# Kernel optimization log

Measured on AMD Instinct MI355X. Metric: run time of the kernel, lower is better.

Reference implementation:

```python
import jax, jax.numpy as jnp
import numpy as np

R_CUT = 2.5
N_BASIS = 8
BOX_SIZE = 10.0


def radial_encode(r, n, r_cut):
    """Gaussian radial basis on squared distance r: (...,) -> (..., n).
    Centers spread over [0, r_cut], width r_cut/n. (Helper source not given;
    this is the standard RBF encode used in such MD graph nets.)"""
    mu = jnp.linspace(0.0, r_cut, n, dtype=r.dtype)        # (n,)
    sigma = r_cut / n
    d = r[..., None] - mu                                   # (..., n)
    return jnp.exp(-0.5 * (d / sigma) ** 2)


def setup_inputs() -> dict:
    key = jax.random.key(0)
    k1, k2 = jax.random.split(key)
    batch, nodes, deg = 8, 20000, 32
    pos = jax.random.uniform(k1, (batch, nodes, 3), dtype=jnp.float32) * BOX_SIZE
    box = jnp.full((3,), BOX_SIZE, dtype=jnp.float32)
    nbr_idx = jax.random.randint(k2, (nodes, deg), 0, nodes, dtype=jnp.int64)
    return {"pos": pos, "box": box, "nbr_idx": nbr_idx}


def reference(pos, box, nbr_idx):
    # pos: (B, N, 3); box: (3,); nbr_idx: (N, deg)
    ang_box = box / (2.0 * jnp.pi)                          # (3,)
    # edges_read: gather neighbor positions -> (B, N, deg, 3)
    nbr_pos = pos[:, nbr_idx]                               # (B, N, deg, 3)
    edges = nbr_pos - pos[:, :, None]                       # relative displacement
    # periodic-box sin wrap
    edges = ang_box * jnp.sin(edges / ang_box)
    r = jnp.sum(edges ** 2, axis=-1)                        # (B, N, deg) squared dist
    x = radial_encode(r, N_BASIS, R_CUT)                    # (B, N, deg, 8)
    xv = x[..., None] * edges[..., None, :]                 # (B, N, deg, 8, 3) outer product
    # edges_reduce: sum over neighbor axis
    y = jnp.sum(x, axis=2)                                  # (B, N, 8)
    yv = jnp.sum(xv, axis=2)                                # (B, N, 8, 3)
    return (y, yv)
```

## Files before the change

### kernel.cpp

```cpp
#include <hip/hip_runtime.h>

static constexpr int BATCH = 8;
static constexpr int NODES = 20000;
static constexpr int DEG   = 32;
static constexpr int NB    = 8;

#if defined(__has_builtin) && __has_builtin(__builtin_amdgcn_exp2f)
#define EXP2F(x) __builtin_amdgcn_exp2f(x)
#else
#define EXP2F(x) exp2f(x)
#endif

static constexpr float C1 = -7.3865986f;
static constexpr float C2 = 5.2761417f;

__global__ __launch_bounds__(256)
void pack_pos_kernel(const float* __restrict__ pos, float4* __restrict__ pos4) {
    const int t = blockIdx.x * blockDim.x + threadIdx.x;
    if (t >= BATCH * NODES) return;
    pos4[t] = make_float4(pos[3 * t + 0], pos[3 * t + 1], pos[3 * t + 2], 0.0f);
}

__global__ __launch_bounds__(256)
void graph_embed_kernel(const float4* __restrict__ pos4,
                        const float* __restrict__ box,
                        const int*   __restrict__ nbr,
                        float* __restrict__ out)
{
    const int t = blockIdx.x * blockDim.x + threadIdx.x;
    if (t >= BATCH * NODES) return;
    const int b = t / NODES;
    const int i = t - b * NODES;

    const float inv2pi = 0.15915494309189535f;
    const float ab0 = box[0] * inv2pi;
    const float ab1 = box[1] * inv2pi;
    const float ab2 = box[2] * inv2pi;
    const float ia0 = 1.0f / ab0;
    const float ia1 = 1.0f / ab1;
    const float ia2 = 1.0f / ab2;

    float h[NB - 1];
#pragma unroll
    for (int k = 0; k < NB - 1; ++k)
        h[k] = __expf(-0.6530612245f * (float)(2 * k + 1));

    const float4* __restrict__ pb = pos4 + (size_t)b * NODES;
    const float4 p = pb[i];

    float y0[NB], v0[NB], v1[NB], v2[NB];
#pragma unroll
    for (int k = 0; k < NB; ++k) { y0[k] = 0.f; v0[k] = 0.f; v1[k] = 0.f; v2[k] = 0.f; }

    const int4* __restrict__ row = (const int4*)(nbr + (size_t)i * DEG);

    int4 idx = row[0];
    float4 q0 = pb[idx.x], q1 = pb[idx.y], q2 = pb[idx.z], q3 = pb[idx.w];

#pragma unroll
    for (int grp = 0; grp < DEG / 4; ++grp) {
        float4 n0, n1, n2, n3;
        if (grp + 1 < DEG / 4) {
            const int4 nidx = row[grp + 1];
            n0 = pb[nidx.x]; n1 = pb[nidx.y]; n2 = pb[nidx.z]; n3 = pb[nidx.w];
        }
        const float4 qs[4] = { q0, q1, q2, q3 };
#pragma unroll
        for (int jj = 0; jj < 4; ++jj) {
            const float4 q = qs[jj];
            const float e0 = ab0 * __sinf((q.x - p.x) * ia0);
            const float e1 = ab1 * __sinf((q.y - p.y) * ia1);
            const float e2 = ab2 * __sinf((q.z - p.z) * ia2);
            const float r  = fmaf(e0, e0, fmaf(e1, e1, e2 * e2));

            const float g = EXP2F(r * C2);
            float x = EXP2F(r * r * C1);
#pragma unroll
            for (int k = 0; k < NB; ++k) {
                y0[k] += x;
                v0[k] = fmaf(x, e0, v0[k]);
                v1[k] = fmaf(x, e1, v1[k]);
                v2[k] = fmaf(x, e2, v2[k]);
                if (k < NB - 1) x = x * g * h[k];
            }
        }
        q0 = n0; q1 = n1; q2 = n2; q3 = n3;
    }

    float* __restrict__ yptr = out + (size_t)t * NB;
    *(float4*)(yptr + 0) = make_float4(y0[0], y0[1], y0[2], y0[3]);
    *(float4*)(yptr + 4) = make_float4(y0[4], y0[5], y0[6], y0[7]);

    float* __restrict__ vptr = out + (size_t)BATCH * NODES * NB + (size_t)t * (NB * 3);
    *(float4*)(vptr +  0) = make_float4(v0[0], v1[0], v2[0], v0[1]);
    *(float4*)(vptr +  4) = make_float4(v1[1], v2[1], v0[2], v1[2]);
    *(float4*)(vptr +  8) = make_float4(v2[2], v0[3], v1[3], v2[3]);
    *(float4*)(vptr + 12) = make_float4(v0[4], v1[4], v2[4], v0[5]);
    *(float4*)(vptr + 16) = make_float4(v1[5], v2[5], v0[6], v1[6]);
    *(float4*)(vptr + 20) = make_float4(v2[6], v0[7], v1[7], v2[7]);
}

__global__ __launch_bounds__(256)
void graph_embed_fallback_kernel(const float* __restrict__ pos,
                                 const float* __restrict__ box,
                                 const int*   __restrict__ nbr,
                                 float* __restrict__ out)
{
    const int t = blockIdx.x * blockDim.x + threadIdx.x;
    if (t >= BATCH * NODES) return;
    const int b = t / NODES;
    const int i = t - b * NODES;

    const float inv2pi = 0.15915494309189535f;
    const float ab0 = box[0] * inv2pi, ab1 = box[1] * inv2pi, ab2 = box[2] * inv2pi;
    const float ia0 = 1.0f / ab0, ia1 = 1.0f / ab1, ia2 = 1.0f / ab2;

    float h[NB - 1];
#pragma unroll
    for (int k = 0; k < NB - 1; ++k)
        h[k] = __expf(-0.6530612245f * (float)(2 * k + 1));

    const float* __restrict__ pb = pos + (size_t)b * NODES * 3;
    const float p0 = pb[3 * i + 0], p1 = pb[3 * i + 1], p2 = pb[3 * i + 2];

    float y0[NB], v0[NB], v1[NB], v2[NB];
#pragma unroll
    for (int k = 0; k < NB; ++k) { y0[k] = 0.f; v0[k] = 0.f; v1[k] = 0.f; v2[k] = 0.f; }

    const int* __restrict__ row = nbr + (size_t)i * DEG;
#pragma unroll 4
    for (int j = 0; j < DEG; ++j) {
        const int idx = row[j];
        const float* __restrict__ q = pb + (size_t)idx * 3;
        const float e0 = ab0 * __sinf((q[0] - p0) * ia0);
        const float e1 = ab1 * __sinf((q[1] - p1) * ia1);
        const float e2 = ab2 * __sinf((q[2] - p2) * ia2);
        const float r  = fmaf(e0, e0, fmaf(e1, e1, e2 * e2));
        const float g = EXP2F(r * C2);
        float x = EXP2F(r * r * C1);
#pragma unroll
        for (int k = 0; k < NB; ++k) {
            y0[k] += x;
            v0[k] = fmaf(x, e0, v0[k]);
            v1[k] = fmaf(x, e1, v1[k]);
            v2[k] = fmaf(x, e2, v2[k]);
            if (k < NB - 1) x = x * g * h[k];
        }
    }

    float* __restrict__ yptr = out + (size_t)t * NB;
    *(float4*)(yptr + 0) = make_float4(y0[0], y0[1], y0[2], y0[3]);
    *(float4*)(yptr + 4) = make_float4(y0[4], y0[5], y0[6], y0[7]);
    float* __restrict__ vptr = out + (size_t)BATCH * NODES * NB + (size_t)t * (NB * 3);
    *(float4*)(vptr +  0) = make_float4(v0[0], v1[0], v2[0], v0[1]);
    *(float4*)(vptr +  4) = make_float4(v1[1], v2[1], v0[2], v1[2]);
    *(float4*)(vptr +  8) = make_float4(v2[2], v0[3], v1[3], v2[3]);
    *(float4*)(vptr + 12) = make_float4(v0[4], v1[4], v2[4], v0[5]);
    *(float4*)(vptr + 16) = make_float4(v1[5], v2[5], v0[6], v1[6]);
    *(float4*)(vptr + 20) = make_float4(v2[6], v0[7], v1[7], v2[7]);
}

extern "C" void kernel_launch(void* const* d_in, const int* in_sizes, int n_in,
                              void* d_out, int out_size, void* d_ws, size_t ws_size,
                              hipStream_t stream) {
    const float* pos = (const float*)d_in[0];
    const float* box = (const float*)d_in[1];
    const int*   nbr = (const int*)d_in[2];
    float* out = (float*)d_out;

    const int total = BATCH * NODES;
    const int block = 256;
    const int grid  = (total + block - 1) / block;

    const size_t packed_bytes = (size_t)total * sizeof(float4);
    if (ws_size >= packed_bytes) {
        float4* pos4 = (float4*)d_ws;
        pack_pos_kernel<<<grid, block, 0, stream>>>(pos, pos4);
        graph_embed_kernel<<<grid, block, 0, stream>>>(pos4, box, nbr, out);
    } else {
        graph_embed_fallback_kernel<<<grid, block, 0, stream>>>(pos, box, nbr, out);
    }
}
```

Before: 100.5 us.

## Interleave batch into node-major position layout and map eight batch threads per node

Positions are repacked as [node][batch] float4, and the thread mapping changes so that eight consecutive threads handle the same node across all batches. Each neighbor gather then reads a contiguous 128-byte run shared by eight lanes, and the neighbor index row is loaded once per group of lanes, which should cut scattered-gather transactions. Output writes are no longer contiguous across adjacent threads, and the transpose kernel's stores are strided, adding some write cost.

Result: faster. 87.96 us (-12.4%).

```diff
diff --git a/kernel.cpp b/kernel.cpp
--- a/kernel.cpp
+++ b/kernel.cpp
@@ -15,22 +15,25 @@
 static constexpr float C2 = 5.2761417f;
 
 __global__ __launch_bounds__(256)
-void pack_pos_kernel(const float* __restrict__ pos, float4* __restrict__ pos4) {
+void transpose_pos_kernel(const float* __restrict__ pos, float4* __restrict__ pos_t) {
     const int t = blockIdx.x * blockDim.x + threadIdx.x;
     if (t >= BATCH * NODES) return;
-    pos4[t] = make_float4(pos[3 * t + 0], pos[3 * t + 1], pos[3 * t + 2], 0.0f);
+    const int b = t / NODES;
+    const int i = t - b * NODES;
+    pos_t[(size_t)i * BATCH + b] =
+        make_float4(pos[3 * t + 0], pos[3 * t + 1], pos[3 * t + 2], 0.0f);
 }
 
 __global__ __launch_bounds__(256)
-void graph_embed_kernel(const float4* __restrict__ pos4,
+void graph_embed_kernel(const float4* __restrict__ pos_t,
                         const float* __restrict__ box,
                         const int*   __restrict__ nbr,
                         float* __restrict__ out)
 {
     const int t = blockIdx.x * blockDim.x + threadIdx.x;
     if (t >= BATCH * NODES) return;
-    const int b = t / NODES;
-    const int i = t - b * NODES;
+    const int i = t >> 3;
+    const int b = t & 7;
 
     const float inv2pi = 0.15915494309189535f;
     const float ab0 = box[0] * inv2pi;
@@ -45,8 +48,7 @@
     for (int k = 0; k < NB - 1; ++k)
         h[k] = __expf(-0.6530612245f * (float)(2 * k + 1));
 
-    const float4* __restrict__ pb = pos4 + (size_t)b * NODES;
-    const float4 p = pb[i];
+    const float4 p = pos_t[(size_t)i * BATCH + b];
 
     float y0[NB], v0[NB], v1[NB], v2[NB];
 #pragma unroll
@@ -55,14 +57,20 @@
     const int4* __restrict__ row = (const int4*)(nbr + (size_t)i * DEG);
 
     int4 idx = row[0];
-    float4 q0 = pb[idx.x], q1 = pb[idx.y], q2 = pb[idx.z], q3 = pb[idx.w];
+    float4 q0 = pos_t[(size_t)idx.x * BATCH + b];
+    float4 q1 = pos_t[(size_t)idx.y * BATCH + b];
+    float4 q2 = pos_t[(size_t)idx.z * BATCH + b];
+    float4 q3 = pos_t[(size_t)idx.w * BATCH + b];
 
 #pragma unroll
     for (int grp = 0; grp < DEG / 4; ++grp) {
         float4 n0, n1, n2, n3;
         if (grp + 1 < DEG / 4) {
             const int4 nidx = row[grp + 1];
-            n0 = pb[nidx.x]; n1 = pb[nidx.y]; n2 = pb[nidx.z]; n3 = pb[nidx.w];
+            n0 = pos_t[(size_t)nidx.x * BATCH + b];
+            n1 = pos_t[(size_t)nidx.y * BATCH + b];
+            n2 = pos_t[(size_t)nidx.z * BATCH + b];
+            n3 = pos_t[(size_t)nidx.w * BATCH + b];
         }
         const float4 qs[4] = { q0, q1, q2, q3 };
 #pragma unroll
@@ -87,11 +95,12 @@
         q0 = n0; q1 = n1; q2 = n2; q3 = n3;
     }
 
-    float* __restrict__ yptr = out + (size_t)t * NB;
+    const size_t ot = (size_t)b * NODES + i;
+    float* __restrict__ yptr = out + ot * NB;
     *(float4*)(yptr + 0) = make_float4(y0[0], y0[1], y0[2], y0[3]);
     *(float4*)(yptr + 4) = make_float4(y0[4], y0[5], y0[6], y0[7]);
 
-    float* __restrict__ vptr = out + (size_t)BATCH * NODES * NB + (size_t)t * (NB * 3);
+    float* __restrict__ vptr = out + (size_t)BATCH * NODES * NB + ot * (NB * 3);
     *(float4*)(vptr +  0) = make_float4(v0[0], v1[0], v2[0], v0[1]);
     *(float4*)(vptr +  4) = make_float4(v1[1], v2[1], v0[2], v1[2]);
     *(float4*)(vptr +  8) = make_float4(v2[2], v0[3], v1[3], v2[3]);
@@ -174,9 +183,9 @@
 
     const size_t packed_bytes = (size_t)total * sizeof(float4);
     if (ws_size >= packed_bytes) {
-        float4* pos4 = (float4*)d_ws;
-        pack_pos_kernel<<<grid, block, 0, stream>>>(pos, pos4);
-        graph_embed_kernel<<<grid, block, 0, stream>>>(pos4, box, nbr, out);
+        float4* pos_t = (float4*)d_ws;
+        transpose_pos_kernel<<<grid, block, 0, stream>>>(pos, pos_t);
+        graph_embed_kernel<<<grid, block, 0, stream>>>(pos_t, box, nbr, out);
     } else {
         graph_embed_fallback_kernel<<<grid, block, 0, stream>>>(pos, box, nbr, out);
     }
```
